# Kernel tuning notes

Hardware: AMD Instinct MI355X
Metric: run time of the kernel (lower is better)

Reference implementation:

```python
import jax, jax.numpy as jnp
import numpy as np

M, K1, N1, N2, N3 = 131072, 256, 1024, 1024, 256


def setup_inputs() -> dict:
    key = jax.random.key(0)
    k_x, k1, k2, k3 = jax.random.split(key, 4)
    x = jax.random.normal(k_x, (M, K1), dtype=jnp.float32)
    # Kaiming-ish scaling so softplus stays in a sane range
    w1 = jax.random.normal(k1, (K1, N1), dtype=jnp.float32) * (1.0 / np.sqrt(K1))
    w2 = jax.random.normal(k2, (N1, N2), dtype=jnp.float32) * (1.0 / np.sqrt(N1))
    w3 = jax.random.normal(k3, (N2, N3), dtype=jnp.float32) * (1.0 / np.sqrt(N2))
    return {"x": x, "w1": w1, "w2": w2, "w3": w3}


def reference(x, w1, w2, w3):
    # Fused 3-layer MLP: out = softplus(softplus(x @ W1) @ W2) @ W3
    h1 = jax.nn.softplus(x @ w1)   # [M, N1]
    h2 = jax.nn.softplus(h1 @ w2)  # [M, N2]
    return h2 @ w3                 # [M, N3]
```

## Files before the change

kernel.cpp:

```cpp
#include <hip/hip_runtime.h>

typedef __attribute__((ext_vector_type(8))) short short8;
typedef __attribute__((ext_vector_type(4))) float floatx4;
typedef __attribute__((ext_vector_type(2))) unsigned int uintx2;
typedef __attribute__((ext_vector_type(4))) unsigned int uintx4;
typedef unsigned short u16;

#define MFMA(a, b, c) __builtin_amdgcn_mfma_f32_16x16x32_bf16((a), (b), (c), 0, 0, 0)

__device__ __forceinline__ u16 f2bf(float f) {
  unsigned int u = __builtin_bit_cast(unsigned int, f);
  u += ((u >> 16) & 1u) + 0x7fffu;
  return (u16)(u >> 16);
}

__device__ __forceinline__ float softplus_f(float v) {
  float a = __builtin_fabsf(v);
  float e = __expf(-a);
  float l = __logf(1.0f + e);
  return __builtin_fmaxf(v, 0.0f) + l;
}

__device__ __forceinline__ unsigned int pack_sp(float lo, float hi) {
  return (unsigned int)f2bf(softplus_f(lo)) | ((unsigned int)f2bf(softplus_f(hi)) << 16);
}

__global__ void transpose_cvt(const float* __restrict__ in, u16* __restrict__ out, int K, int N) {
  __shared__ float tile[32][33];
  const int bn = blockIdx.x * 32, bk = blockIdx.y * 32;
  const int tx = threadIdx.x, ty = threadIdx.y;
#pragma unroll
  for (int i = 0; i < 32; i += 8)
    tile[ty + i][tx] = in[(size_t)(bk + ty + i) * N + bn + tx];
  __syncthreads();
#pragma unroll
  for (int i = 0; i < 32; i += 8)
    out[(size_t)(bn + ty + i) * K + bk + tx] = f2bf(tile[tx][ty + i]);
}

__global__ void cvt_bf16_kernel(const float* __restrict__ in, u16* __restrict__ out, long n8) {
  long i = (long)blockIdx.x * blockDim.x + threadIdx.x;
  const long stride = (long)gridDim.x * blockDim.x;
  for (; i < n8; i += stride) {
    floatx4 a = ((const floatx4*)in)[2 * i], b = ((const floatx4*)in)[2 * i + 1];
    uintx4 o;
    o.x = (unsigned)f2bf(a.x) | ((unsigned)f2bf(a.y) << 16);
    o.y = (unsigned)f2bf(a.z) | ((unsigned)f2bf(a.w) << 16);
    o.z = (unsigned)f2bf(b.x) | ((unsigned)f2bf(b.y) << 16);
    o.w = (unsigned)f2bf(b.z) | ((unsigned)f2bf(b.w) << 16);
    ((uintx4*)out)[i] = o;
  }
}


__device__ __forceinline__ void gld16(const void* g, void* l) {
  __builtin_amdgcn_global_load_lds((const __attribute__((address_space(1))) void*)g,
                                   (__attribute__((address_space(3))) void*)l, 16, 0, 0);
}

__device__ __forceinline__ void stage_half(const u16* __restrict__ gsrc, size_t row0, int K,
                                           int kof, u16* halfp, int wv, int lane) {
#pragma unroll
  for (int j = 0; j < 2; ++j) {
    const int G = (wv * 2 + j) * 64 + lane;
    const int r = G >> 2;
    const int g = (G & 3) ^ (r & 3);
    gld16(gsrc + (row0 + (size_t)r) * K + kof + g * 8, halfp + (wv * 2 + j) * 512);
  }
}

__device__ __forceinline__ short8 rdfrag(const u16* half_, int r, int g) {
  return *(const short8*)(half_ + (r * 4 + (g ^ (r & 3))) * 8);
}

#define PHASE(B, KH, NH, FRESH, STOP, STKH, STBUF, STTILE, DOVM)                              \
  {                                                                                           \
    if (FRESH) {                                                                              \
      _Pragma("unroll") for (int mt = 0; mt < 8; ++mt)                                        \
          bf[mt] = rdfrag(&lds[B][0][KH][0], wvm * 128 + mt * 16 + l15, g);                   \
    }                                                                                         \
    af[0] = rdfrag(&lds[B][1][KH][0], wvn * 64 + (NH)*32 + l15, g);                           \
    af[1] = rdfrag(&lds[B][1][KH][0], wvn * 64 + (NH)*32 + 16 + l15, g);                      \
    if ((STOP) == 0)                                                                          \
      stage_half(act, am0, K, (STTILE)*64 + (STKH)*32, &lds[STBUF][0][STKH][0], wv, lane);    \
    else                                                                                      \
      stage_half(wt, wn0, K, (STTILE)*64 + (STKH)*32, &lds[STBUF][1][STKH][0], wv, lane);     \
    if (DOVM) asm volatile("s_waitcnt vmcnt(8)" ::: "memory");                                \
    asm volatile("" ::: "memory");                                                            \
    __builtin_amdgcn_s_barrier();                                                             \
    asm volatile("" ::: "memory");                                                            \
    __builtin_amdgcn_s_setprio(1);                                                            \
    _Pragma("unroll") for (int mt = 0; mt < 8; ++mt) {                                        \
      acc[(NH)*2 + 0][mt] = MFMA(af[0], bf[mt], acc[(NH)*2 + 0][mt]);                         \
      acc[(NH)*2 + 1][mt] = MFMA(af[1], bf[mt], acc[(NH)*2 + 1][mt]);                         \
    }                                                                                         \
    __builtin_amdgcn_s_setprio(0);                                                            \
    asm volatile("" ::: "memory");                                                            \
    __builtin_amdgcn_s_barrier();                                                             \
    asm volatile("" ::: "memory");                                                            \
  }

template <int K, int EPI>
__global__ __launch_bounds__(512, 2) void gemm8p(const u16* __restrict__ act,
                                                 const u16* __restrict__ wt,
                                                 void* __restrict__ Cout, int N, int nbn) {
  __shared__ u16 lds[2][2][2][8192];
  const int tid = threadIdx.x, lane = tid & 63, wv = tid >> 6;
  const int l15 = lane & 15, g = lane >> 4;
  const int wvm = wv >> 2, wvn = wv & 3;
  const int nwg = gridDim.x, o = blockIdx.x;
  const int sw = (o & 7) * (nwg >> 3) + (o >> 3);
  const int bm = sw / nbn, bn = sw % nbn;
  const size_t am0 = (size_t)bm * 256;
  const size_t wn0 = (size_t)bn * 256;
  constexpr int NT = K / 64, NIT = NT / 2;

  floatx4 acc[4][8];
  const floatx4 z4 = {0.f, 0.f, 0.f, 0.f};
#pragma unroll
  for (int t = 0; t < 4; ++t)
#pragma unroll
    for (int mt = 0; mt < 8; ++mt) acc[t][mt] = z4;

  stage_half(act, am0, K, 0, &lds[0][0][0][0], wv, lane);
  stage_half(wt, wn0, K, 0, &lds[0][1][0][0], wv, lane);
  stage_half(act, am0, K, 32, &lds[0][0][1][0], wv, lane);
  stage_half(wt, wn0, K, 32, &lds[0][1][1][0], wv, lane);
  stage_half(act, am0, K, 64, &lds[1][0][0][0], wv, lane);
  stage_half(wt, wn0, K, 64, &lds[1][1][0][0], wv, lane);
  asm volatile("s_waitcnt vmcnt(0)" ::: "memory");
  __builtin_amdgcn_s_barrier();
  asm volatile("" ::: "memory");

  short8 bf[8], af[2];
#pragma unroll 1
  for (int it = 0; it < NIT; ++it) {
    const int s01 = 2 * it + 1;
    const int s25 = (2 * it + 2 < NT - 1) ? 2 * it + 2 : NT - 1;
    const int s67 = (2 * it + 3 < NT - 1) ? 2 * it + 3 : NT - 1;
    PHASE(0, 0, 0, true,  0, 1, 1, s01, false)
    PHASE(0, 0, 1, false, 1, 1, 1, s01, true)
    PHASE(0, 1, 0, true,  0, 0, 0, s25, false)
    PHASE(0, 1, 1, false, 1, 0, 0, s25, true)
    PHASE(1, 0, 0, true,  0, 1, 0, s25, false)
    PHASE(1, 0, 1, false, 1, 1, 0, s25, true)
    PHASE(1, 1, 0, true,  0, 0, 1, s67, false)
    PHASE(1, 1, 1, false, 1, 0, 1, s67, true)
  }

#pragma unroll
  for (int t = 0; t < 4; ++t)
#pragma unroll
    for (int mt = 0; mt < 8; ++mt) {
      const size_t m = am0 + wvm * 128 + mt * 16 + l15;
      const int n = (int)wn0 + wvn * 64 + t * 16 + g * 4;
      if (EPI == 0) {
        uintx2 pk;
        pk.x = pack_sp(acc[t][mt].x, acc[t][mt].y);
        pk.y = pack_sp(acc[t][mt].z, acc[t][mt].w);
        *(uintx2*)((u16*)Cout + m * N + n) = pk;
      } else {
        *(floatx4*)((float*)Cout + m * N + n) = acc[t][mt];
      }
    }
}

__global__ __launch_bounds__(512, 2) void mlp3_fused(const float* __restrict__ x,
                                                     const u16* __restrict__ w1t,
                                                     const u16* __restrict__ w2t,
                                                     const u16* __restrict__ w3t,
                                                     float* __restrict__ out) {
  __shared__ u16 h1s[64 * 1024];
  __shared__ u16 xs[64 * 256];
  const int tid = threadIdx.x, lane = tid & 63, wv = tid >> 6;
  const int l15 = lane & 15, g = lane >> 4;
  const size_t m0 = (size_t)blockIdx.x * 64;
  const floatx4 z4 = {0.f, 0.f, 0.f, 0.f};
  {
    const float* xp = x + m0 * 256;
#pragma unroll
    for (int r = 0; r < 8; ++r) {
      int idx4 = r * 512 + tid;
      int m = idx4 >> 6, k = (idx4 & 63) << 2;
      floatx4 v = *(const floatx4*)(xp + m * 256 + k);
      uintx2 pk;
      pk.x = (unsigned)f2bf(v.x) | ((unsigned)f2bf(v.y) << 16);
      pk.y = (unsigned)f2bf(v.z) | ((unsigned)f2bf(v.w) << 16);
      *(uintx2*)(xs + ((m * 256 + k) ^ ((m & 7) << 3))) = pk;
    }
  }
  __syncthreads();
#pragma unroll 1
  for (int c = 0; c < 4; ++c) {
    floatx4 acc[2][4];
#pragma unroll
    for (int t = 0; t < 2; ++t)
#pragma unroll
      for (int mt = 0; mt < 4; ++mt) acc[t][mt] = z4;
    const u16* p0 = w1t + (size_t)(c * 256 + wv * 32 + l15) * 256;
#pragma unroll
    for (int ks = 0; ks < 8; ++ks) {
      const int k = ks * 32 + g * 8;
      short8 a0 = *(const short8*)(p0 + k);
      short8 a1 = *(const short8*)(p0 + 16 * 256 + k);
      short8 b0 = *(const short8*)(xs + (((0 * 16 + l15) * 256 + k) ^ ((l15 & 7) << 3)));
      short8 b1 = *(const short8*)(xs + (((1 * 16 + l15) * 256 + k) ^ ((l15 & 7) << 3)));
      short8 b2 = *(const short8*)(xs + (((2 * 16 + l15) * 256 + k) ^ ((l15 & 7) << 3)));
      short8 b3 = *(const short8*)(xs + (((3 * 16 + l15) * 256 + k) ^ ((l15 & 7) << 3)));
      acc[0][0] = MFMA(a0, b0, acc[0][0]); acc[0][1] = MFMA(a0, b1, acc[0][1]);
      acc[0][2] = MFMA(a0, b2, acc[0][2]); acc[0][3] = MFMA(a0, b3, acc[0][3]);
      acc[1][0] = MFMA(a1, b0, acc[1][0]); acc[1][1] = MFMA(a1, b1, acc[1][1]);
      acc[1][2] = MFMA(a1, b2, acc[1][2]); acc[1][3] = MFMA(a1, b3, acc[1][3]);
    }
#pragma unroll
    for (int t = 0; t < 2; ++t)
#pragma unroll
      for (int mt = 0; mt < 4; ++mt) {
        const int n1 = c * 256 + wv * 32 + t * 16 + g * 4;
        const int m = mt * 16 + l15;
        uintx2 pk;
        pk.x = pack_sp(acc[t][mt].x, acc[t][mt].y);
        pk.y = pack_sp(acc[t][mt].z, acc[t][mt].w);
        *(uintx2*)(h1s + ((m * 1024 + n1) ^ ((m & 7) << 3))) = pk;
      }
  }
  __syncthreads();
  floatx4 acc3[2][4];
#pragma unroll
  for (int t = 0; t < 2; ++t)
#pragma unroll
    for (int mt = 0; mt < 4; ++mt) acc3[t][mt] = z4;
#pragma unroll 1
  for (int c2 = 0; c2 < 4; ++c2) {
    floatx4 acc2[2][4];
#pragma unroll
    for (int t = 0; t < 2; ++t)
#pragma unroll
      for (int mt = 0; mt < 4; ++mt) acc2[t][mt] = z4;
    {
      const u16* p0 = w2t + (size_t)(c2 * 256 + wv * 32 + l15) * 1024;
#pragma unroll 4
      for (int ks = 0; ks < 32; ++ks) {
        const int k = ks * 32 + g * 8;
        short8 a0 = *(const short8*)(p0 + k);
        short8 a1 = *(const short8*)(p0 + 16 * 1024 + k);
        short8 b0 = *(const short8*)(h1s + (((0 * 16 + l15) * 1024 + k) ^ ((l15 & 7) << 3)));
        short8 b1 = *(const short8*)(h1s + (((1 * 16 + l15) * 1024 + k) ^ ((l15 & 7) << 3)));
        short8 b2 = *(const short8*)(h1s + (((2 * 16 + l15) * 1024 + k) ^ ((l15 & 7) << 3)));
        short8 b3 = *(const short8*)(h1s + (((3 * 16 + l15) * 1024 + k) ^ ((l15 & 7) << 3)));
        acc2[0][0] = MFMA(a0, b0, acc2[0][0]); acc2[0][1] = MFMA(a0, b1, acc2[0][1]);
        acc2[0][2] = MFMA(a0, b2, acc2[0][2]); acc2[0][3] = MFMA(a0, b3, acc2[0][3]);
        acc2[1][0] = MFMA(a1, b0, acc2[1][0]); acc2[1][1] = MFMA(a1, b1, acc2[1][1]);
        acc2[1][2] = MFMA(a1, b2, acc2[1][2]); acc2[1][3] = MFMA(a1, b3, acc2[1][3]);
      }
    }
    __syncthreads();
#pragma unroll
    for (int t = 0; t < 2; ++t)
#pragma unroll
      for (int mt = 0; mt < 4; ++mt) {
        const int n2l = wv * 32 + t * 16 + g * 4;
        const int m = mt * 16 + l15;
        uintx2 pk;
        pk.x = pack_sp(acc2[t][mt].x, acc2[t][mt].y);
        pk.y = pack_sp(acc2[t][mt].z, acc2[t][mt].w);
        *(uintx2*)(xs + ((m * 256 + n2l) ^ ((m & 7) << 3))) = pk;
      }
    __syncthreads();
    {
      const u16* p0 = w3t + (size_t)(wv * 32 + l15) * 1024 + c2 * 256;
#pragma unroll
      for (int ks = 0; ks < 8; ++ks) {
        const int k = ks * 32 + g * 8;
        short8 a0 = *(const short8*)(p0 + k);
        short8 a1 = *(const short8*)(p0 + 16 * 1024 + k);
        short8 b0 = *(const short8*)(xs + (((0 * 16 + l15) * 256 + k) ^ ((l15 & 7) << 3)));
        short8 b1 = *(const short8*)(xs + (((1 * 16 + l15) * 256 + k) ^ ((l15 & 7) << 3)));
        short8 b2 = *(const short8*)(xs + (((2 * 16 + l15) * 256 + k) ^ ((l15 & 7) << 3)));
        short8 b3 = *(const short8*)(xs + (((3 * 16 + l15) * 256 + k) ^ ((l15 & 7) << 3)));
        acc3[0][0] = MFMA(a0, b0, acc3[0][0]); acc3[0][1] = MFMA(a0, b1, acc3[0][1]);
        acc3[0][2] = MFMA(a0, b2, acc3[0][2]); acc3[0][3] = MFMA(a0, b3, acc3[0][3]);
        acc3[1][0] = MFMA(a1, b0, acc3[1][0]); acc3[1][1] = MFMA(a1, b1, acc3[1][1]);
        acc3[1][2] = MFMA(a1, b2, acc3[1][2]); acc3[1][3] = MFMA(a1, b3, acc3[1][3]);
      }
    }
  }
#pragma unroll
  for (int t = 0; t < 2; ++t)
#pragma unroll
    for (int mt = 0; mt < 4; ++mt) {
      const int n3 = wv * 32 + t * 16 + g * 4;
      const int m = mt * 16 + l15;
      *(floatx4*)(out + (m0 + m) * 256 + n3) = acc3[t][mt];
    }
}

extern "C" void kernel_launch(void* const* d_in, const int* in_sizes, int n_in,
                              void* d_out, int out_size, void* d_ws, size_t ws_size,
                              hipStream_t stream) {
  const float* x = (const float*)d_in[0];
  const float* w1 = (const float*)d_in[1];
  const float* w2 = (const float*)d_in[2];
  const float* w3 = (const float*)d_in[3];
  float* out = (float*)d_out;
  const size_t M = 131072;

  u16* w1t = (u16*)d_ws;
  u16* w2t = w1t + 1024 * 256;
  u16* w3t = w2t + 1024 * 1024;
  u16* bufA = w3t + 256 * 1024;
  const size_t weights_el = 1024 * 256 + 1024 * 1024 + 256 * 1024;

  size_t CM = 0;
  const size_t cands[4] = {32768, 16384, 8192, 4096};
  for (int i = 0; i < 4; ++i) {
    size_t need = (weights_el + 2 * cands[i] * 1024) * sizeof(u16);
    if (ws_size >= need) { CM = cands[i]; break; }
  }

  dim3 tb(32, 8);
  transpose_cvt<<<dim3(32, 8), tb, 0, stream>>>(w1, w1t, 256, 1024);
  transpose_cvt<<<dim3(32, 32), tb, 0, stream>>>(w2, w2t, 1024, 1024);
  transpose_cvt<<<dim3(8, 32), tb, 0, stream>>>(w3, w3t, 1024, 256);

  if (CM) {
    u16* bufB = bufA + CM * 1024;
    const int nchunk = (int)(M / CM);
    for (int ci = 0; ci < nchunk; ++ci) {
      const float* xc = x + (size_t)ci * CM * 256;
      float* oc = out + (size_t)ci * CM * 256;
      cvt_bf16_kernel<<<1024, 256, 0, stream>>>(xc, bufA, (long)(CM * 32));
      gemm8p<256, 0><<<(int)(CM / 256) * 4, 512, 0, stream>>>(bufA, w1t, bufB, 1024, 4);
      gemm8p<1024, 0><<<(int)(CM / 256) * 4, 512, 0, stream>>>(bufB, w2t, bufA, 1024, 4);
      gemm8p<1024, 1><<<(int)(CM / 256), 512, 0, stream>>>(bufA, w3t, oc, 256, 1);
    }
  } else {
    mlp3_fused<<<M / 64, 512, 0, stream>>>(x, w1t, w2t, w3t, out);
  }
}
```

Before: 702.2 us.

## Stage GEMM epilogue through swizzled LDS for coalesced stores; retune swizzle and load order

The GEMM epilogue now writes accumulator tiles into LDS using an XOR swizzle, then reads them back so each thread stores full 16-byte contiguous row segments to global memory. Previously each lane wrote scattered 8- or 16-byte fragments. The LDS swizzle for operand staging changes from keying on row&3 to (row>>1)&3 to reduce bank conflicts. The global-to-LDS stage is issued before the fragment reads so the loads overlap earlier. The epilogue adds barriers and an extra LDS round trip, and it only helps if the gemm8p path runs rather than the fused kernel.

```diff
diff --git a/kernel.cpp b/kernel.cpp
--- a/kernel.cpp
+++ b/kernel.cpp
@@ -64,27 +64,27 @@
   for (int j = 0; j < 2; ++j) {
     const int G = (wv * 2 + j) * 64 + lane;
     const int r = G >> 2;
-    const int g = (G & 3) ^ (r & 3);
+    const int g = (G & 3) ^ ((r >> 1) & 3);
     gld16(gsrc + (row0 + (size_t)r) * K + kof + g * 8, halfp + (wv * 2 + j) * 512);
   }
 }
 
 __device__ __forceinline__ short8 rdfrag(const u16* half_, int r, int g) {
-  return *(const short8*)(half_ + (r * 4 + (g ^ (r & 3))) * 8);
+  return *(const short8*)(half_ + (r * 4 + (g ^ ((r >> 1) & 3))) * 8);
 }
 
 #define PHASE(B, KH, NH, FRESH, STOP, STKH, STBUF, STTILE, DOVM)                              \
   {                                                                                           \
+    if ((STOP) == 0)                                                                          \
+      stage_half(act, am0, K, (STTILE)*64 + (STKH)*32, &lds[STBUF][0][STKH][0], wv, lane);    \
+    else                                                                                      \
+      stage_half(wt, wn0, K, (STTILE)*64 + (STKH)*32, &lds[STBUF][1][STKH][0], wv, lane);     \
     if (FRESH) {                                                                              \
       _Pragma("unroll") for (int mt = 0; mt < 8; ++mt)                                        \
           bf[mt] = rdfrag(&lds[B][0][KH][0], wvm * 128 + mt * 16 + l15, g);                   \
     }                                                                                         \
     af[0] = rdfrag(&lds[B][1][KH][0], wvn * 64 + (NH)*32 + l15, g);                           \
     af[1] = rdfrag(&lds[B][1][KH][0], wvn * 64 + (NH)*32 + 16 + l15, g);                      \
-    if ((STOP) == 0)                                                                          \
-      stage_half(act, am0, K, (STTILE)*64 + (STKH)*32, &lds[STBUF][0][STKH][0], wv, lane);    \
-    else                                                                                      \
-      stage_half(wt, wn0, K, (STTILE)*64 + (STKH)*32, &lds[STBUF][1][STKH][0], wv, lane);     \
     if (DOVM) asm volatile("s_waitcnt vmcnt(8)" ::: "memory");                                \
     asm volatile("" ::: "memory");                                                            \
     __builtin_amdgcn_s_barrier();                                                             \
@@ -148,21 +148,59 @@
     PHASE(1, 1, 1, false, 1, 0, 1, s67, true)
   }
 
-#pragma unroll
-  for (int t = 0; t < 4; ++t)
-#pragma unroll
-    for (int mt = 0; mt < 8; ++mt) {
-      const size_t m = am0 + wvm * 128 + mt * 16 + l15;
-      const int n = (int)wn0 + wvn * 64 + t * 16 + g * 4;
-      if (EPI == 0) {
+  asm volatile("s_waitcnt vmcnt(0)" ::: "memory");
+  __builtin_amdgcn_s_barrier();
+
+  if (EPI == 0) {
+    u16* cl = &lds[0][0][0][0];
+#pragma unroll
+    for (int t = 0; t < 4; ++t)
+#pragma unroll
+      for (int mt = 0; mt < 8; ++mt) {
+        const int m = wvm * 128 + mt * 16 + l15;
+        const int n0 = wvn * 64 + t * 16 + g * 4;
+        const int j = n0 >> 3, h = (n0 >> 2) & 1;
         uintx2 pk;
         pk.x = pack_sp(acc[t][mt].x, acc[t][mt].y);
         pk.y = pack_sp(acc[t][mt].z, acc[t][mt].w);
-        *(uintx2*)((u16*)Cout + m * N + n) = pk;
-      } else {
-        *(floatx4*)((float*)Cout + m * N + n) = acc[t][mt];
-      }
-    }
+        *(uintx2*)(cl + m * 256 + ((j ^ (m & 7)) << 3) + (h << 2)) = pk;
+      }
+    __syncthreads();
+    u16* outp = (u16*)Cout;
+#pragma unroll
+    for (int i = 0; i < 16; ++i) {
+      const int c = i * 512 + tid;
+      const int m = c >> 5, j = c & 31;
+      uintx4 v = *(const uintx4*)(cl + m * 256 + ((j ^ (m & 7)) << 3));
+      *(uintx4*)(outp + (am0 + m) * N + wn0 + j * 8) = v;
+    }
+  } else {
+    float* cf = (float*)&lds[0][0][0][0];
+#pragma unroll
+    for (int hm = 0; hm < 2; ++hm) {
+      if (hm) __syncthreads();
+      if (wvm == hm) {
+#pragma unroll
+        for (int t = 0; t < 4; ++t)
+#pragma unroll
+          for (int mt = 0; mt < 8; ++mt) {
+            const int m = mt * 16 + l15;
+            const int p = (wvn * 64 + t * 16 + g * 4) >> 1;
+            *(floatx4*)(cf + m * 256 + ((p ^ ((m & 7) << 1)) << 1)) = acc[t][mt];
+          }
+      }
+      __syncthreads();
+      float* outp = (float*)Cout;
+#pragma unroll
+      for (int i = 0; i < 16; ++i) {
+        const int c = i * 512 + tid;
+        const int m = c >> 6;
+        const int p = (c & 63) * 2;
+        floatx4 v = *(const floatx4*)(cf + m * 256 + ((p ^ ((m & 7) << 1)) << 1));
+        *(floatx4*)(outp + (am0 + hm * 128 + m) * N + wn0 + (c & 63) * 4) = v;
+      }
+    }
+  }
 }
 
 __global__ __launch_bounds__(512, 2) void mlp3_fused(const float* __restrict__ x,
```

After: 703.1 us. Within noise of the previous version (+0.1%).
